# Performance work log

Hardware: AMD Instinct MI355X
Metric: run time of the kernel (lower is better)

## Reference

```python
import jax, jax.numpy as jnp
import numpy as np

# geomloss SamplesLoss(loss='sinkhorn', p=2, reach=1.0, blur=0.1) constants
P = 2
BLUR = 0.1
REACH = 1.0
SCALING = 0.5
EPS_FINAL = BLUR ** P          # 0.01
RHO = REACH ** P               # 1.0
DIAMETER = 2.0 * np.sqrt(2.0)  # PMT positions scaled to [-1,1]^2


def eps_schedule():
    # geomloss epsilon_schedule(p, diameter, blur, scaling)
    e = [DIAMETER ** P]
    for t in np.arange(P * np.log(DIAMETER), P * np.log(BLUR), P * np.log(SCALING)):
        e.append(float(np.exp(t)))
    e.append(BLUR ** P)
    return [float(v) for v in e]


def _softmin(eps, C, h):
    # h: (B, N) log-measure + potential/eps ; C: (N, N) shared cost -> (B, N)
    return -eps * jax.scipy.special.logsumexp(h[:, None, :] - C[None, :, :] / eps, axis=-1)


def _sinkhorn_potentials(a_log, b_log, C):
    # symmetric unbalanced Sinkhorn loop with eps-annealing (geomloss sinkhorn_loop)
    eps_list = eps_schedule()
    damp = lambda eps: 1.0 / (1.0 + eps / RHO)
    eps0 = eps_list[0]
    d0 = damp(eps0)
    g_ab = d0 * _softmin(eps0, C, a_log)
    f_ba = d0 * _softmin(eps0, C, b_log)
    f_aa = d0 * _softmin(eps0, C, a_log)
    g_bb = d0 * _softmin(eps0, C, b_log)
    for eps in eps_list:
        d = damp(eps)
        ft = d * _softmin(eps, C, b_log + g_ab / eps)
        gt = d * _softmin(eps, C, a_log + f_ba / eps)
        f_ba, g_ab = 0.5 * (f_ba + ft), 0.5 * (g_ab + gt)
        f_aa = 0.5 * (f_aa + d * _softmin(eps, C, a_log + f_aa / eps))
        g_bb = 0.5 * (g_bb + d * _softmin(eps, C, b_log + g_bb / eps))
    # last extrapolation at the final (target) temperature
    eps = eps_list[-1]
    d = damp(eps)
    f_ba, g_ab = (d * _softmin(eps, C, b_log + g_ab / eps),
                  d * _softmin(eps, C, a_log + f_ba / eps))
    f_aa = d * _softmin(eps, C, a_log + f_aa / eps)
    g_bb = d * _softmin(eps, C, b_log + g_bb / eps)
    return f_aa, g_bb, g_ab, f_ba


def setup_inputs() -> dict:
    key = jax.random.key(0)
    k1, k2, k3 = jax.random.split(key, 3)
    B, N = 32768, 32
    # positive PE weights (measure masses must be > 0 for log-domain Sinkhorn)
    pred_pmtpe = jax.random.uniform(k1, (B, N), jnp.float32, 0.05, 1.0)
    target_pe = jax.random.uniform(k2, (B, N), jnp.float32, 0.05, 1.0)
    # fixed scaled 2D (z,y) PMT layout in [-1,1]^2, shared by pred and target clouds
    pmt_pos = jax.random.uniform(k3, (N, 2), jnp.float32, -1.0, 1.0)
    batchstart = jnp.arange(B, dtype=jnp.int64) * N
    batchend = batchstart + N
    return {"pred_pmtpe": pred_pmtpe, "target_pe": target_pe, "pmt_pos": pmt_pos,
            "batchstart": batchstart, "batchend": batchend}


def reference(pred_pmtpe, target_pe, pmt_pos, batchstart, batchend):
    # shared cost matrix (x_pred_batch == y_target_batch == PMT layout), C = |x-y|^2/2 for p=2
    C = 0.5 * jnp.sum((pmt_pos[:, None, :] - pmt_pos[None, :, :]) ** 2, axis=-1)  # (32,32)
    # geomloss runs the Sinkhorn loop with autograd disabled (envelope theorem)
    a_log = jnp.log(jax.lax.stop_gradient(pred_pmtpe))
    b_log = jnp.log(jax.lax.stop_gradient(target_pe))
    f_aa, g_bb, g_ab, f_ba = _sinkhorn_potentials(a_log, b_log, C)
    f_aa, g_bb, g_ab, f_ba = map(jax.lax.stop_gradient, (f_aa, g_bb, g_ab, f_ba))
    # unbalanced debiased sinkhorn cost (geomloss sinkhorn_cost, rho finite)
    eps = EPS_FINAL
    scale = RHO + 0.5 * eps
    per_batch = scale * (
        jnp.sum(pred_pmtpe * (jnp.exp(-f_aa / RHO) - jnp.exp(-f_ba / RHO)), axis=-1)
        + jnp.sum(target_pe * (jnp.exp(-g_bb / RHO) - jnp.exp(-g_ab / RHO)), axis=-1)
    )
    return jnp.mean(per_batch)
```

## Files before the change

### kernel.cpp

```cpp
#include <hip/hip_runtime.h>
#include <hip/hip_bf16.h>

#define EXP2F(x)  __builtin_amdgcn_exp2f(x)
#define LOG2FD(x) __builtin_amdgcn_logf(x)
#define L2E 1.4426950408889634f
#define T1F 1.2621774e-29f

typedef __attribute__((ext_vector_type(8))) short bf16x8;
typedef __attribute__((ext_vector_type(4))) float f32x4;
typedef __attribute__((ext_vector_type(2))) unsigned int u32x2;

#define MFMA16(A, B, C) __builtin_amdgcn_mfma_f32_16x16x32_bf16((A), (B), (C), 0, 0, 0)

union U8 { unsigned int u[4]; bf16x8 v; };
union U8S { unsigned short s[8]; bf16x8 v; };

__device__ __forceinline__ void split_pack(const float* w, bf16x8& hi, bf16x8& lo) {
  U8 a, b;
#pragma unroll
  for (int k = 0; k < 4; ++k) {
    float x0 = w[2*k], x1 = w[2*k+1];
    unsigned u0 = __float_as_uint(x0) & 0xFFFF0000u;
    unsigned u1 = __float_as_uint(x1) & 0xFFFF0000u;
    float r0 = x0 - __uint_as_float(u0);
    float r1 = x1 - __uint_as_float(u1);
    a.u[k] = (u0 >> 16) | u1;
    b.u[k] = ((__float_as_uint(r0) & 0xFFFF0000u) >> 16) |
             (__float_as_uint(r1) & 0xFFFF0000u);
  }
  hi = a.v; lo = b.v;
}

__device__ __forceinline__ bf16x8 pack_bf16(const float* w) {
  U8S a;
#pragma unroll
  for (int e = 0; e < 8; ++e) {
    __hip_bfloat16 b = __float2bfloat16(w[e]);
    a.s[e] = reinterpret_cast<const unsigned short&>(b);
  }
  return a.v;
}

__device__ __forceinline__ float pmax32(float v) {
  u32x2 r = __builtin_amdgcn_permlane32_swap(__float_as_uint(v), __float_as_uint(v),
                                             false, false);
  return fmaxf(__uint_as_float(r.x), __uint_as_float(r.y));
}

__device__ __forceinline__ void buildK(const float* c2a, const float* c2b, float inv,
                                       bf16x8& KA1, bf16x8& KA2, bf16x8& KB1, bf16x8& KB2) {
  float ka[8], kb[8];
#pragma unroll
  for (int e = 0; e < 8; ++e) { ka[e] = EXP2F(-c2a[e] * inv); kb[e] = EXP2F(-c2b[e] * inv); }
  split_pack(ka, KA1, KA2);
  split_pack(kb, KB1, KB2);
}

__device__ __forceinline__ void pot_assign(float* pot, const float* Ts, int b15, int g) {
  float4 r0 = *(const float4*)&Ts[b15*36 + 8*g];
  float4 r1 = *(const float4*)&Ts[b15*36 + 8*g + 4];
  pot[0]=r0.x; pot[1]=r0.y; pot[2]=r0.z; pot[3]=r0.w;
  pot[4]=r1.x; pot[5]=r1.y; pot[6]=r1.z; pot[7]=r1.w;
}

__device__ __forceinline__ void pot_merge(float* pot, const float* Ts, int b15, int g) {
  float4 r0 = *(const float4*)&Ts[b15*36 + 8*g];
  float4 r1 = *(const float4*)&Ts[b15*36 + 8*g + 4];
  pot[0]=0.5f*(pot[0]+r0.x); pot[1]=0.5f*(pot[1]+r0.y);
  pot[2]=0.5f*(pot[2]+r0.z); pot[3]=0.5f*(pot[3]+r0.w);
  pot[4]=0.5f*(pot[4]+r1.x); pot[5]=0.5f*(pot[5]+r1.y);
  pot[6]=0.5f*(pot[6]+r1.z); pot[7]=0.5f*(pot[7]+r1.w);
}

__device__ __noinline__ float exact_lse(const float2* pos2, const float* HB,
                                        int i, float inv) {
  float2 pi = pos2[i];
  float m = -3.4e38f;
#pragma unroll 1
  for (int j = 0; j < 32; ++j) {
    float2 pj = pos2[j];
    float dx = pi.x - pj.x, dy = pi.y - pj.y;
    float arg = fmaf((0.5f*L2E)*(dx*dx + dy*dy), -inv, HB[j]);
    m = fmaxf(m, arg);
  }
  float s = 0.f;
#pragma unroll 1
  for (int j = 0; j < 32; ++j) {
    float2 pj = pos2[j];
    float dx = pi.x - pj.x, dy = pi.y - pj.y;
    float arg = fmaf((0.5f*L2E)*(dx*dx + dy*dy), -inv, HB[j]);
    s += EXP2F(arg - m);
  }
  return m + LOG2FD(s);
}

template<int NQ, bool CHECKED>
__device__ __forceinline__ void ksoft_multi(float* Ts, float* Hdump,
    const float Hq[][8], bf16x8 KA1, bf16x8 KA2, bf16x8 KB1, bf16x8 KB2,
    float nde, float inv, int b15, int g, const float2* pos2) {
  float hm[NQ], d[NQ][8];
  bf16x8 w1[NQ];
#pragma unroll
  for (int q = 0; q < NQ; ++q) {
    const float* H = Hq[q];
    float m = fmaxf(fmaxf(fmaxf(H[0], H[1]), fmaxf(H[2], H[3])),
                    fmaxf(fmaxf(H[4], H[5]), fmaxf(H[6], H[7])));
    m = fmaxf(m, __shfl_xor(m, 16));
    m = pmax32(m);
    hm[q] = m;
    float w[8];
#pragma unroll
    for (int e = 0; e < 8; ++e) { d[q][e] = H[e] - m; w[e] = EXP2F(d[q][e]); }
    w1[q] = pack_bf16(w);
  }
  f32x4 a0[NQ], a1[NQ];
  const f32x4 z = {0.f, 0.f, 0.f, 0.f};
#pragma unroll
  for (int q = 0; q < NQ; ++q) { a0[q] = MFMA16(KA1, w1[q], z);     a1[q] = MFMA16(KB1, w1[q], z); }
#pragma unroll
  for (int q = 0; q < NQ; ++q) { a0[q] = MFMA16(KA2, w1[q], a0[q]); a1[q] = MFMA16(KB2, w1[q], a1[q]); }
#pragma unroll
  for (int q = 0; q < NQ; ++q) {
    float r0[4], r1[4];
#pragma unroll
    for (int r = 0; r < 4; ++r) {
      r0[r] = hm[q] + LOG2FD(a0[q][r]);
      r1[r] = hm[q] + LOG2FD(a1[q][r]);
    }
    if (CHECKED) {
      float mn = fminf(fminf(fminf(a0[q][0], a0[q][1]), fminf(a0[q][2], a0[q][3])),
                       fminf(fminf(a1[q][0], a1[q][1]), fminf(a1[q][2], a1[q][3])));
      if (__any(mn < T1F)) {
        float wb[8];
#pragma unroll
        for (int e = 0; e < 8; ++e) wb[e] = EXP2F(d[q][e] + 96.f);
        bf16x8 u1 = pack_bf16(wb);
        f32x4 b0 = MFMA16(KA1, u1, z);
        b0 = MFMA16(KA2, u1, b0);
        f32x4 b1 = MFMA16(KB1, u1, z);
        b1 = MFMA16(KB2, u1, b1);
        bool mybad = false;
#pragma unroll
        for (int r = 0; r < 4; ++r) {
          if (a0[q][r] < T1F) r0[r] = (hm[q] - 96.f) + LOG2FD(b0[r]);
          if (a1[q][r] < T1F) r1[r] = (hm[q] - 96.f) + LOG2FD(b1[r]);
          mybad |= (a0[q][r] < T1F) && (b0[r] < T1F);
          mybad |= (a1[q][r] < T1F) && (b1[r] < T1F);
        }
        if (__any(mybad)) {
          float4 h0 = {Hq[q][0], Hq[q][1], Hq[q][2], Hq[q][3]};
          float4 h1 = {Hq[q][4], Hq[q][5], Hq[q][6], Hq[q][7]};
          *(float4*)&Hdump[b15*36 + 8*g]     = h0;
          *(float4*)&Hdump[b15*36 + 8*g + 4] = h1;
          asm volatile("" ::: "memory");
          const float* HB = &Hdump[b15*36];
#pragma unroll
          for (int r = 0; r < 4; ++r) {
            if ((a0[q][r] < T1F) && (b0[r] < T1F)) r0[r] = exact_lse(pos2, HB, 4*g + r, inv);
            if ((a1[q][r] < T1F) && (b1[r] < T1F)) r1[r] = exact_lse(pos2, HB, 16 + 4*g + r, inv);
          }
        }
      }
    }
    float4 v0 = {nde*r0[0], nde*r0[1], nde*r0[2], nde*r0[3]};
    float4 v1 = {nde*r1[0], nde*r1[1], nde*r1[2], nde*r1[3]};
    float* Tq = Ts + q * 576;
    *(float4*)&Tq[b15*36 + 4*g]      = v0;
    *(float4*)&Tq[b15*36 + 4*g + 16] = v1;
  }
}

__global__ __launch_bounds__(64, 2) void sink_kernel(
    const float* __restrict__ pred, const float* __restrict__ tgt,
    const float* __restrict__ pos, float* __restrict__ ws) {
  __shared__ __align__(16) float sT[4][576];
  __shared__ __align__(16) float sHb[16][36];

  const int lid = threadIdx.x;
  const int b15 = lid & 15;
  const int g   = lid >> 4;
  const int bbase = blockIdx.x * 16;
  const float2* pos2 = (const float2*)pos;
  float* Tw = &sT[0][0];
  float* Hd = &sHb[0][0];

  float al2[8], bl2[8];
  {
    const float* pr = &pred[(bbase + b15) * 32 + 8 * g];
    const float* tr = &tgt [(bbase + b15) * 32 + 8 * g];
    float4 p0 = *(const float4*)&pr[0];
    float4 p1 = *(const float4*)&pr[4];
    float4 t0 = *(const float4*)&tr[0];
    float4 t1 = *(const float4*)&tr[4];
    al2[0]=LOG2FD(p0.x); al2[1]=LOG2FD(p0.y); al2[2]=LOG2FD(p0.z); al2[3]=LOG2FD(p0.w);
    al2[4]=LOG2FD(p1.x); al2[5]=LOG2FD(p1.y); al2[6]=LOG2FD(p1.z); al2[7]=LOG2FD(p1.w);
    bl2[0]=LOG2FD(t0.x); bl2[1]=LOG2FD(t0.y); bl2[2]=LOG2FD(t0.z); bl2[3]=LOG2FD(t0.w);
    bl2[4]=LOG2FD(t1.x); bl2[5]=LOG2FD(t1.y); bl2[6]=LOG2FD(t1.z); bl2[7]=LOG2FD(t1.w);
  }
  float c2a[8], c2b[8];
  {
    float2 pm0 = pos2[b15];
    float2 pm1 = pos2[b15 + 16];
#pragma unroll
    for (int e = 0; e < 8; ++e) {
      float2 pj = pos2[8*g + e];
      float dx0 = pm0.x - pj.x, dy0 = pm0.y - pj.y;
      float dx1 = pm1.x - pj.x, dy1 = pm1.y - pj.y;
      c2a[e] = (0.5f*L2E)*(dx0*dx0 + dy0*dy0);
      c2b[e] = (0.5f*L2E)*(dx1*dx1 + dy1*dy1);
    }
  }

  bf16x8 KA1, KA2, KB1, KB2;
  float Fba[8], Gab[8], Faa[8], Gbb[8];

  buildK(c2a, c2b, 0.125f, KA1, KA2, KB1, KB2);
  {
    float Hq[2][8];
#pragma unroll
    for (int e = 0; e < 8; ++e) { Hq[0][e] = bl2[e]; Hq[1][e] = al2[e]; }
    ksoft_multi<2, false>(Tw, Hd, Hq, KA1, KA2, KB1, KB2, -8.f/9.f, 0.125f, b15, g, pos2);
  }
  pot_assign(Fba, Tw + 0*576, b15, g);
  pot_assign(Gab, Tw + 1*576, b15, g);
#pragma unroll
  for (int e = 0; e < 8; ++e) { Faa[e] = Gab[e]; Gbb[e] = Fba[e]; }

  const float INV[8] = {0.125f, 0.125f, 0.5f, 2.f, 8.f, 32.f, 100.f, 100.f};
  const float NDE[8] = {-8.f/9.f, -8.f/9.f, -2.f/3.f, -1.f/3.f, -1.f/9.f,
                        -1.f/33.f, -1.f/101.f, -1.f/101.f};

#pragma unroll
  for (int k = 0; k < 5; ++k) {
    const float inv = INV[k], nde = NDE[k];
    float Hq[4][8];
#pragma unroll
    for (int e = 0; e < 8; ++e) {
      Hq[0][e] = fmaf(Gab[e], inv, bl2[e]);
      Hq[1][e] = fmaf(Fba[e], inv, al2[e]);
      Hq[2][e] = fmaf(Faa[e], inv, al2[e]);
      Hq[3][e] = fmaf(Gbb[e], inv, bl2[e]);
    }
    ksoft_multi<4, false>(Tw, Hd, Hq, KA1, KA2, KB1, KB2, nde, inv, b15, g, pos2);
    if (INV[k+1] != inv)
      buildK(c2a, c2b, INV[k+1], KA1, KA2, KB1, KB2);
    pot_merge(Fba, Tw + 0*576, b15, g);
    pot_merge(Gab, Tw + 1*576, b15, g);
    pot_merge(Faa, Tw + 2*576, b15, g);
    pot_merge(Gbb, Tw + 3*576, b15, g);
  }

#pragma unroll
  for (int k = 5; k < 8; ++k) {
    const float inv = INV[k], nde = NDE[k];
    const bool avg = (k < 7);
    float Hq[4][8];
#pragma unroll
    for (int e = 0; e < 8; ++e) {
      Hq[0][e] = fmaf(Gab[e], inv, bl2[e]);
      Hq[1][e] = fmaf(Fba[e], inv, al2[e]);
      Hq[2][e] = fmaf(Faa[e], inv, al2[e]);
      Hq[3][e] = fmaf(Gbb[e], inv, bl2[e]);
    }
    ksoft_multi<4, true>(Tw, Hd, Hq, KA1, KA2, KB1, KB2, nde, inv, b15, g, pos2);
    if (k < 7 && INV[k+1] != inv)
      buildK(c2a, c2b, INV[k+1], KA1, KA2, KB1, KB2);
    if (avg) {
      pot_merge(Fba, Tw + 0*576, b15, g);
      pot_merge(Gab, Tw + 1*576, b15, g);
      pot_merge(Faa, Tw + 2*576, b15, g);
      pot_merge(Gbb, Tw + 3*576, b15, g);
    } else {
      pot_assign(Fba, Tw + 0*576, b15, g);
      pot_assign(Gab, Tw + 1*576, b15, g);
      pot_assign(Faa, Tw + 2*576, b15, g);
      pot_assign(Gbb, Tw + 3*576, b15, g);
    }
  }

  float c = 0.f;
#pragma unroll
  for (int e = 0; e < 8; ++e) {
    c += EXP2F(al2[e]) * (EXP2F(-Faa[e]) - EXP2F(-Fba[e]))
       + EXP2F(bl2[e]) * (EXP2F(-Gbb[e]) - EXP2F(-Gab[e]));
  }
  c += __shfl_xor(c, 1);
  c += __shfl_xor(c, 2);
  c += __shfl_xor(c, 4);
  c += __shfl_xor(c, 8);
  c += __shfl_xor(c, 16);
  c += __shfl_xor(c, 32);
  if (lid == 0) ws[blockIdx.x] = c;
}

__global__ __launch_bounds__(256) void reduce_kernel(
    const float* __restrict__ ws, float* __restrict__ out, int n, float scale) {
  float s = 0.f;
  for (int i = threadIdx.x; i < n; i += 256) s += ws[i];
  s += __shfl_xor(s, 32);
  s += __shfl_xor(s, 16);
  s += __shfl_xor(s, 8);
  s += __shfl_xor(s, 4);
  s += __shfl_xor(s, 2);
  s += __shfl_xor(s, 1);
  __shared__ float a[4];
  if ((threadIdx.x & 63) == 0) a[threadIdx.x >> 6] = s;
  __syncthreads();
  if (threadIdx.x == 0) out[0] = ((a[0] + a[1]) + (a[2] + a[3])) * scale;
}

extern "C" void kernel_launch(void* const* d_in, const int* in_sizes, int n_in,
                              void* d_out, int out_size, void* d_ws, size_t ws_size,
                              hipStream_t stream) {
  const float* pred = (const float*)d_in[0];
  const float* tgt  = (const float*)d_in[1];
  const float* pos  = (const float*)d_in[2];
  const int B = in_sizes[0] / 32;
  const int nblocks = B / 16;
  float* ws = (float*)d_ws;

  sink_kernel<<<nblocks, 64, 0, stream>>>(pred, tgt, pos, ws);
  reduce_kernel<<<1, 256, 0, stream>>>(ws, (float*)d_out, nblocks,
                                       1.005f / (float)B);
}
```

Measured before the change: 26.08 us.

## Process two 16-batch groups per wavefront with eight softmin streams

Each 64-thread block now handles 32 batch rows instead of 16. Both 16-row groups are interleaved through a single 8-stream ksoft_multi call, which halves the block count and shares the K-matrix construction across twice the work. The iteration loops are no longer unrolled, to bound code size, and launch bounds drop to one block per SIMD hint. The rare exact-fallback path now dumps the shifted d+hm values rather than the original Hq. Register pressure and LDS use double, and there are fewer blocks to hide latency.

```diff
diff --git a/kernel.cpp b/kernel.cpp
--- a/kernel.cpp
+++ b/kernel.cpp
@@ -148,8 +148,8 @@
           mybad |= (a1[q][r] < T1F) && (b1[r] < T1F);
         }
         if (__any(mybad)) {
-          float4 h0 = {Hq[q][0], Hq[q][1], Hq[q][2], Hq[q][3]};
-          float4 h1 = {Hq[q][4], Hq[q][5], Hq[q][6], Hq[q][7]};
+          float4 h0 = {d[q][0]+hm[q], d[q][1]+hm[q], d[q][2]+hm[q], d[q][3]+hm[q]};
+          float4 h1 = {d[q][4]+hm[q], d[q][5]+hm[q], d[q][6]+hm[q], d[q][7]+hm[q]};
           *(float4*)&Hdump[b15*36 + 8*g]     = h0;
           *(float4*)&Hdump[b15*36 + 8*g + 4] = h1;
           asm volatile("" ::: "memory");
@@ -170,32 +170,33 @@
   }
 }
 
-__global__ __launch_bounds__(64, 2) void sink_kernel(
+__global__ __launch_bounds__(64, 1) void sink_kernel(
     const float* __restrict__ pred, const float* __restrict__ tgt,
     const float* __restrict__ pos, float* __restrict__ ws) {
-  __shared__ __align__(16) float sT[4][576];
+  __shared__ __align__(16) float sT[8][576];
   __shared__ __align__(16) float sHb[16][36];
 
   const int lid = threadIdx.x;
   const int b15 = lid & 15;
   const int g   = lid >> 4;
-  const int bbase = blockIdx.x * 16;
+  const int bbase = blockIdx.x * 32;
   const float2* pos2 = (const float2*)pos;
   float* Tw = &sT[0][0];
   float* Hd = &sHb[0][0];
 
-  float al2[8], bl2[8];
-  {
-    const float* pr = &pred[(bbase + b15) * 32 + 8 * g];
-    const float* tr = &tgt [(bbase + b15) * 32 + 8 * g];
+  float al2[2][8], bl2[2][8];
+#pragma unroll
+  for (int u = 0; u < 2; ++u) {
+    const float* pr = &pred[(bbase + 16*u + b15) * 32 + 8 * g];
+    const float* tr = &tgt [(bbase + 16*u + b15) * 32 + 8 * g];
     float4 p0 = *(const float4*)&pr[0];
     float4 p1 = *(const float4*)&pr[4];
     float4 t0 = *(const float4*)&tr[0];
     float4 t1 = *(const float4*)&tr[4];
-    al2[0]=LOG2FD(p0.x); al2[1]=LOG2FD(p0.y); al2[2]=LOG2FD(p0.z); al2[3]=LOG2FD(p0.w);
-    al2[4]=LOG2FD(p1.x); al2[5]=LOG2FD(p1.y); al2[6]=LOG2FD(p1.z); al2[7]=LOG2FD(p1.w);
-    bl2[0]=LOG2FD(t0.x); bl2[1]=LOG2FD(t0.y); bl2[2]=LOG2FD(t0.z); bl2[3]=LOG2FD(t0.w);
-    bl2[4]=LOG2FD(t1.x); bl2[5]=LOG2FD(t1.y); bl2[6]=LOG2FD(t1.z); bl2[7]=LOG2FD(t1.w);
+    al2[u][0]=LOG2FD(p0.x); al2[u][1]=LOG2FD(p0.y); al2[u][2]=LOG2FD(p0.z); al2[u][3]=LOG2FD(p0.w);
+    al2[u][4]=LOG2FD(p1.x); al2[u][5]=LOG2FD(p1.y); al2[u][6]=LOG2FD(p1.z); al2[u][7]=LOG2FD(p1.w);
+    bl2[u][0]=LOG2FD(t0.x); bl2[u][1]=LOG2FD(t0.y); bl2[u][2]=LOG2FD(t0.z); bl2[u][3]=LOG2FD(t0.w);
+    bl2[u][4]=LOG2FD(t1.x); bl2[u][5]=LOG2FD(t1.y); bl2[u][6]=LOG2FD(t1.z); bl2[u][7]=LOG2FD(t1.w);
   }
   float c2a[8], c2b[8];
   {
@@ -212,78 +213,96 @@
   }
 
   bf16x8 KA1, KA2, KB1, KB2;
-  float Fba[8], Gab[8], Faa[8], Gbb[8];
+  float Fba[2][8], Gab[2][8], Faa[2][8], Gbb[2][8];
 
   buildK(c2a, c2b, 0.125f, KA1, KA2, KB1, KB2);
   {
-    float Hq[2][8];
-#pragma unroll
-    for (int e = 0; e < 8; ++e) { Hq[0][e] = bl2[e]; Hq[1][e] = al2[e]; }
-    ksoft_multi<2, false>(Tw, Hd, Hq, KA1, KA2, KB1, KB2, -8.f/9.f, 0.125f, b15, g, pos2);
-  }
-  pot_assign(Fba, Tw + 0*576, b15, g);
-  pot_assign(Gab, Tw + 1*576, b15, g);
-#pragma unroll
-  for (int e = 0; e < 8; ++e) { Faa[e] = Gab[e]; Gbb[e] = Fba[e]; }
+    float Hq[4][8];
+#pragma unroll
+    for (int e = 0; e < 8; ++e) {
+      Hq[0][e] = bl2[0][e]; Hq[1][e] = al2[0][e];
+      Hq[2][e] = bl2[1][e]; Hq[3][e] = al2[1][e];
+    }
+    ksoft_multi<4, false>(Tw, Hd, Hq, KA1, KA2, KB1, KB2, -8.f/9.f, 0.125f, b15, g, pos2);
+  }
+#pragma unroll
+  for (int u = 0; u < 2; ++u) {
+    pot_assign(Fba[u], Tw + (2*u + 0)*576, b15, g);
+    pot_assign(Gab[u], Tw + (2*u + 1)*576, b15, g);
+#pragma unroll
+    for (int e = 0; e < 8; ++e) { Faa[u][e] = Gab[u][e]; Gbb[u][e] = Fba[u][e]; }
+  }
 
   const float INV[8] = {0.125f, 0.125f, 0.5f, 2.f, 8.f, 32.f, 100.f, 100.f};
   const float NDE[8] = {-8.f/9.f, -8.f/9.f, -2.f/3.f, -1.f/3.f, -1.f/9.f,
                         -1.f/33.f, -1.f/101.f, -1.f/101.f};
 
-#pragma unroll
+#pragma unroll 1
   for (int k = 0; k < 5; ++k) {
     const float inv = INV[k], nde = NDE[k];
-    float Hq[4][8];
-#pragma unroll
-    for (int e = 0; e < 8; ++e) {
-      Hq[0][e] = fmaf(Gab[e], inv, bl2[e]);
-      Hq[1][e] = fmaf(Fba[e], inv, al2[e]);
-      Hq[2][e] = fmaf(Faa[e], inv, al2[e]);
-      Hq[3][e] = fmaf(Gbb[e], inv, bl2[e]);
-    }
-    ksoft_multi<4, false>(Tw, Hd, Hq, KA1, KA2, KB1, KB2, nde, inv, b15, g, pos2);
+    float Hq[8][8];
+#pragma unroll
+    for (int u = 0; u < 2; ++u)
+#pragma unroll
+      for (int e = 0; e < 8; ++e) {
+        Hq[4*u+0][e] = fmaf(Gab[u][e], inv, bl2[u][e]);
+        Hq[4*u+1][e] = fmaf(Fba[u][e], inv, al2[u][e]);
+        Hq[4*u+2][e] = fmaf(Faa[u][e], inv, al2[u][e]);
+        Hq[4*u+3][e] = fmaf(Gbb[u][e], inv, bl2[u][e]);
+      }
+    ksoft_multi<8, false>(Tw, Hd, Hq, KA1, KA2, KB1, KB2, nde, inv, b15, g, pos2);
     if (INV[k+1] != inv)
       buildK(c2a, c2b, INV[k+1], KA1, KA2, KB1, KB2);
-    pot_merge(Fba, Tw + 0*576, b15, g);
-    pot_merge(Gab, Tw + 1*576, b15, g);
-    pot_merge(Faa, Tw + 2*576, b15, g);
-    pot_merge(Gbb, Tw + 3*576, b15, g);
-  }
-
-#pragma unroll
+#pragma unroll
+    for (int u = 0; u < 2; ++u) {
+      pot_merge(Fba[u], Tw + (4*u+0)*576, b15, g);
+      pot_merge(Gab[u], Tw + (4*u+1)*576, b15, g);
+      pot_merge(Faa[u], Tw + (4*u+2)*576, b15, g);
+      pot_merge(Gbb[u], Tw + (4*u+3)*576, b15, g);
+    }
+  }
+
+#pragma unroll 1
   for (int k = 5; k < 8; ++k) {
     const float inv = INV[k], nde = NDE[k];
     const bool avg = (k < 7);
-    float Hq[4][8];
+    float Hq[8][8];
+#pragma unroll
+    for (int u = 0; u < 2; ++u)
+#pragma unroll
+      for (int e = 0; e < 8; ++e) {
+        Hq[4*u+0][e] = fmaf(Gab[u][e], inv, bl2[u][e]);
+        Hq[4*u+1][e] = fmaf(Fba[u][e], inv, al2[u][e]);
+        Hq[4*u+2][e] = fmaf(Faa[u][e], inv, al2[u][e]);
+        Hq[4*u+3][e] = fmaf(Gbb[u][e], inv, bl2[u][e]);
+      }
+    ksoft_multi<8, true>(Tw, Hd, Hq, KA1, KA2, KB1, KB2, nde, inv, b15, g, pos2);
+    if (k == 5)
+      buildK(c2a, c2b, 100.f, KA1, KA2, KB1, KB2);
+#pragma unroll
+    for (int u = 0; u < 2; ++u) {
+      if (avg) {
+        pot_merge(Fba[u], Tw + (4*u+0)*576, b15, g);
+        pot_merge(Gab[u], Tw + (4*u+1)*576, b15, g);
+        pot_merge(Faa[u], Tw + (4*u+2)*576, b15, g);
+        pot_merge(Gbb[u], Tw + (4*u+3)*576, b15, g);
+      } else {
+        pot_assign(Fba[u], Tw + (4*u+0)*576, b15, g);
+        pot_assign(Gab[u], Tw + (4*u+1)*576, b15, g);
+        pot_assign(Faa[u], Tw + (4*u+2)*576, b15, g);
+        pot_assign(Gbb[u], Tw + (4*u+3)*576, b15, g);
+      }
+    }
+  }
+
+  float c = 0.f;
+#pragma unroll
+  for (int u = 0; u < 2; ++u)
 #pragma unroll
     for (int e = 0; e < 8; ++e) {
-      Hq[0][e] = fmaf(Gab[e], inv, bl2[e]);
-      Hq[1][e] = fmaf(Fba[e], inv, al2[e]);
-      Hq[2][e] = fmaf(Faa[e], inv, al2[e]);
-      Hq[3][e] = fmaf(Gbb[e], inv, bl2[e]);
-    }
-    ksoft_multi<4, true>(Tw, Hd, Hq, KA1, KA2, KB1, KB2, nde, inv, b15, g, pos2);
-    if (k < 7 && INV[k+1] != inv)
-      buildK(c2a, c2b, INV[k+1], KA1, KA2, KB1, KB2);
-    if (avg) {
-      pot_merge(Fba, Tw + 0*576, b15, g);
-      pot_merge(Gab, Tw + 1*576, b15, g);
-      pot_merge(Faa, Tw + 2*576, b15, g);
-      pot_merge(Gbb, Tw + 3*576, b15, g);
-    } else {
-      pot_assign(Fba, Tw + 0*576, b15, g);
-      pot_assign(Gab, Tw + 1*576, b15, g);
-      pot_assign(Faa, Tw + 2*576, b15, g);
-      pot_assign(Gbb, Tw + 3*576, b15, g);
-    }
-  }
-
-  float c = 0.f;
-#pragma unroll
-  for (int e = 0; e < 8; ++e) {
-    c += EXP2F(al2[e]) * (EXP2F(-Faa[e]) - EXP2F(-Fba[e]))
-       + EXP2F(bl2[e]) * (EXP2F(-Gbb[e]) - EXP2F(-Gab[e]));
-  }
+      c += EXP2F(al2[u][e]) * (EXP2F(-Faa[u][e]) - EXP2F(-Fba[u][e]))
+         + EXP2F(bl2[u][e]) * (EXP2F(-Gbb[u][e]) - EXP2F(-Gab[u][e]));
+    }
   c += __shfl_xor(c, 1);
   c += __shfl_xor(c, 2);
   c += __shfl_xor(c, 4);
@@ -316,7 +335,7 @@
   const float* tgt  = (const float*)d_in[1];
   const float* pos  = (const float*)d_in[2];
   const int B = in_sizes[0] / 32;
-  const int nblocks = B / 16;
+  const int nblocks = B / 32;
   float* ws = (float*)d_ws;
 
   sink_kernel<<<nblocks, 64, 0, stream>>>(pred, tgt, pos, ws);
```

After: 29.00 us. 11.2% more time.
